# Kernel tuning notes

Measured on AMD Instinct MI355X. Metric: run time of the kernel, lower is better.

## Reference

```python
import jax, jax.numpy as jnp
import numpy as np

B, T, D = 4, 2048, 2048
N_HEADS, N_KV = 16, 4
HEAD_DIM = D // N_HEADS  # 128
N_REP = N_HEADS // N_KV
THETA = 10000.0


def _rope_cos_sin(seq_len, dim, theta):
    inv_freq = 1.0 / (theta ** (jnp.arange(0, dim, 2, dtype=jnp.float32) / dim))
    t = jnp.arange(seq_len, dtype=jnp.float32)
    freqs = jnp.outer(t, inv_freq)               # [T, dim/2]
    emb = jnp.concatenate([freqs, freqs], -1)    # [T, dim]
    return jnp.cos(emb)[None, None], jnp.sin(emb)[None, None]  # [1,1,T,dim]


def _rotate_half(x):
    x1, x2 = jnp.split(x, 2, axis=-1)
    return jnp.concatenate([-x2, x1], axis=-1)


def setup_inputs() -> dict:
    key = jax.random.key(0)
    ks = jax.random.split(key, 5)
    x = jax.random.normal(ks[0], (B, T, D), dtype=jnp.float32)
    # additive causal mask
    causal = jnp.tril(jnp.ones((T, T), dtype=bool))
    mask = jnp.where(causal, 0.0, -1e9).astype(jnp.float32)[None, None]
    s = 0.02
    wq = jax.random.normal(ks[1], (D, N_HEADS * HEAD_DIM), dtype=jnp.float32) * s
    wk = jax.random.normal(ks[2], (D, N_KV * HEAD_DIM), dtype=jnp.float32) * s
    wv = jax.random.normal(ks[3], (D, N_KV * HEAD_DIM), dtype=jnp.float32) * s
    wo = jax.random.normal(ks[4], (D, D), dtype=jnp.float32) * s
    return {"x": x, "mask": mask, "wq": wq, "wk": wk, "wv": wv, "wo": wo}


def reference(x, mask, wq, wk, wv, wo):
    Bc, Tc, _ = x.shape
    q = (x @ wq).reshape(Bc, Tc, N_HEADS, HEAD_DIM).transpose(0, 2, 1, 3)  # [B,H,T,hd]
    k = (x @ wk).reshape(Bc, Tc, N_KV, HEAD_DIM).transpose(0, 2, 1, 3)     # [B,Kv,T,hd]
    v = (x @ wv).reshape(Bc, Tc, N_KV, HEAD_DIM).transpose(0, 2, 1, 3)

    cos, sin = _rope_cos_sin(Tc, HEAD_DIM, THETA)
    q = q * cos + _rotate_half(q) * sin
    k = k * cos + _rotate_half(k) * sin

    # repeat kv heads: [B,Kv,T,hd] -> [B,Kv*n_rep,T,hd]
    k = jnp.repeat(k, N_REP, axis=1)
    v = jnp.repeat(v, N_REP, axis=1)

    scale = HEAD_DIM ** -0.5
    attn = jnp.einsum("bhqd,bhkd->bhqk", q, k) * scale
    attn = attn + mask
    attn = jax.nn.softmax(attn, axis=-1)
    out = jnp.einsum("bhqk,bhkd->bhqd", attn, v)  # [B,H,T,hd]
    out = out.transpose(0, 2, 1, 3).reshape(Bc, Tc, -1)
    return out @ wo
```

## Files before the change

### kernel.cpp

```cpp
#include <hip/hip_runtime.h>

typedef __bf16 bf16;
typedef float  f32x4  __attribute__((ext_vector_type(4)));
typedef float  f32x2  __attribute__((ext_vector_type(2)));
typedef float  f32x16 __attribute__((ext_vector_type(16)));
typedef __bf16 bf16x8 __attribute__((ext_vector_type(8)));
typedef __bf16 bf16x4 __attribute__((ext_vector_type(4)));
typedef unsigned short ushort4_ __attribute__((ext_vector_type(4)));
typedef unsigned int   uint2_   __attribute__((ext_vector_type(2)));

typedef unsigned int __attribute__((address_space(1))) uint_g;
typedef unsigned int __attribute__((address_space(3))) uint_l;

#define DEV __device__ __forceinline__

DEV void gload16(const void* g, void* l) {
  __builtin_amdgcn_global_load_lds((uint_g*)g, (uint_l*)l, 16, 0, 0);
}

#define PHASE_SYNC do { \
  asm volatile("s_barrier" ::: "memory"); \
  asm volatile("s_waitcnt lgkmcnt(0)" ::: "memory"); \
  __builtin_amdgcn_sched_barrier(0); } while (0)

__global__ void k_cvt(const float* __restrict__ in, bf16* __restrict__ out) {
  int i = blockIdx.x * 256 + threadIdx.x;
  f32x4 v = *((const f32x4*)in + i);
  bf16x4 o;
  o[0] = (bf16)v[0]; o[1] = (bf16)v[1]; o[2] = (bf16)v[2]; o[3] = (bf16)v[3];
  *((bf16x4*)out + i) = o;
}

__global__ void k_transpose_cvt(const float* __restrict__ in, bf16* __restrict__ out,
                                int K, int N) {
  __shared__ bf16 tile[64][65];
  int n0 = blockIdx.x * 64, k0 = blockIdx.y * 64;
  int tx = threadIdx.x & 63, ty = threadIdx.x >> 6;
#pragma unroll
  for (int r = 0; r < 64; r += 4)
    tile[r + ty][tx] = (bf16)in[(size_t)(k0 + r + ty) * N + n0 + tx];
  __syncthreads();
#pragma unroll
  for (int r = 0; r < 64; r += 4)
    out[(size_t)(n0 + r + ty) * K + k0 + tx] = tile[tx][r + ty];
}

__global__ void k_rope_tab(f32x2* __restrict__ tab) {
  int idx = blockIdx.x * 256 + threadIdx.x;
  int t = idx >> 6, i = idx & 63;
  float inv = powf(10000.f, -(float)i * (1.f / 64.f));
  float ang = (float)t * inv;
  f32x2 cs; cs[0] = cosf(ang); cs[1] = sinf(ang);
  tab[idx] = cs;
}

template <int MODE>
__global__ __launch_bounds__(512, 2) void k_gemm256(const bf16* __restrict__ A,
                                                    const bf16* __restrict__ Bt,
                                                    void* __restrict__ Cq,
                                                    bf16* __restrict__ Ck,
                                                    bf16* __restrict__ Cv,
                                                    int K) {
  __shared__ bf16 Asm[2][256 * 64];
  __shared__ bf16 Bsm[2][256 * 64];
  const int tid = threadIdx.x;
  const int w = tid >> 6, l = tid & 63, lr = l & 15, lg = l >> 4;
  const int wr = w >> 2, wc = w & 3;
  const int bn = blockIdx.x, bm = blockIdx.y;

  const int srow = tid >> 3;
  const int scb = ((tid & 7) << 4) ^ ((srow & 7) << 4);
  const bf16* Ag = A  + ((size_t)(bm * 256) + srow) * K;
  const bf16* Bg = Bt + ((size_t)(bn * 256) + srow) * K;
  const int ldsbase = w << 10;

  auto stA = [&](int buf, int s, int k0) {
    gload16((const char*)Ag + ((size_t)(s * 64) * K + k0) * 2 + scb,
            (char*)&Asm[buf][0] + s * 8192 + ldsbase);
  };
  auto stB = [&](int buf, int s, int k0) {
    gload16((const char*)Bg + ((size_t)(s * 64) * K + k0) * 2 + scb,
            (char*)&Bsm[buf][0] + s * 8192 + ldsbase);
  };
  auto ldA = [&](int buf, int mf, int kk) -> bf16x8 {
    int row = wr * 128 + mf * 16 + lr;
    return *(const bf16x8*)((const char*)&Asm[buf][0] + row * 128 +
                            ((kk * 64 + lg * 16) ^ ((lr & 7) << 4)));
  };
  auto ldB = [&](int buf, int nf, int kk) -> bf16x8 {
    int row = wc * 64 + nf * 16 + lr;
    return *(const bf16x8*)((const char*)&Bsm[buf][0] + row * 128 +
                            ((kk * 64 + lg * 16) ^ ((lr & 7) << 4)));
  };

  f32x4 acc[8][4] = {};
  const int nt = K >> 6;

#pragma unroll
  for (int s = 0; s < 4; s++) { stA(0, s, 0); stB(0, s, 0); }
  asm volatile("s_waitcnt vmcnt(0)" ::: "memory");
  __syncthreads();

#pragma unroll 1
  for (int t = 0; t < nt; t++) {
    const int cur = t & 1, nxt = cur ^ 1;
    const int kn = (t + 1) << 6;
    const bool pre = (t + 1 < nt);
    bf16x8 a0[4][2], a1[4][2], b0[2][2], b1[2][2];

#pragma unroll
    for (int mf = 0; mf < 4; mf++) { a0[mf][0] = ldA(cur, mf, 0); a0[mf][1] = ldA(cur, mf, 1); }
#pragma unroll
    for (int nf = 0; nf < 2; nf++) { b0[nf][0] = ldB(cur, nf, 0); b0[nf][1] = ldB(cur, nf, 1); }
    if (pre) { stA(nxt, 0, kn); stA(nxt, 1, kn); stA(nxt, 2, kn); }
    PHASE_SYNC;
    __builtin_amdgcn_s_setprio(1);
#pragma unroll
    for (int mf = 0; mf < 4; mf++)
#pragma unroll
      for (int nf = 0; nf < 2; nf++)
#pragma unroll
        for (int kk = 0; kk < 2; kk++)
          acc[mf][nf] = __builtin_amdgcn_mfma_f32_16x16x32_bf16(a0[mf][kk], b0[nf][kk], acc[mf][nf], 0, 0, 0);
    __builtin_amdgcn_s_setprio(0);

#pragma unroll
    for (int nf = 0; nf < 2; nf++) { b1[nf][0] = ldB(cur, nf + 2, 0); b1[nf][1] = ldB(cur, nf + 2, 1); }
    if (pre) { stA(nxt, 3, kn); stB(nxt, 0, kn); stB(nxt, 1, kn); }
    PHASE_SYNC;
    __builtin_amdgcn_s_setprio(1);
#pragma unroll
    for (int mf = 0; mf < 4; mf++)
#pragma unroll
      for (int nf = 0; nf < 2; nf++)
#pragma unroll
        for (int kk = 0; kk < 2; kk++)
          acc[mf][nf + 2] = __builtin_amdgcn_mfma_f32_16x16x32_bf16(a0[mf][kk], b1[nf][kk], acc[mf][nf + 2], 0, 0, 0);
    __builtin_amdgcn_s_setprio(0);

#pragma unroll
    for (int mf = 0; mf < 4; mf++) { a1[mf][0] = ldA(cur, mf + 4, 0); a1[mf][1] = ldA(cur, mf + 4, 1); }
    if (pre) { stB(nxt, 2, kn); stB(nxt, 3, kn); }
    PHASE_SYNC;
    __builtin_amdgcn_s_setprio(1);
#pragma unroll
    for (int mf = 0; mf < 4; mf++)
#pragma unroll
      for (int nf = 0; nf < 2; nf++)
#pragma unroll
        for (int kk = 0; kk < 2; kk++)
          acc[mf + 4][nf] = __builtin_amdgcn_mfma_f32_16x16x32_bf16(a1[mf][kk], b0[nf][kk], acc[mf + 4][nf], 0, 0, 0);
    __builtin_amdgcn_s_setprio(0);

    __builtin_amdgcn_s_setprio(1);
#pragma unroll
    for (int mf = 0; mf < 4; mf++)
#pragma unroll
      for (int nf = 0; nf < 2; nf++)
#pragma unroll
        for (int kk = 0; kk < 2; kk++)
          acc[mf + 4][nf + 2] = __builtin_amdgcn_mfma_f32_16x16x32_bf16(a1[mf][kk], b1[nf][kk], acc[mf + 4][nf + 2], 0, 0, 0);
    __builtin_amdgcn_s_setprio(0);
    asm volatile("s_waitcnt vmcnt(0)" ::: "memory");
    asm volatile("s_barrier" ::: "memory");
  }

#pragma unroll
  for (int mf = 0; mf < 8; mf++) {
    const int rowb = bm * 256 + wr * 128 + mf * 16 + lg * 4;
#pragma unroll
    for (int nf = 0; nf < 4; nf++) {
      const int col = bn * 256 + wc * 64 + nf * 16 + lr;
      if constexpr (MODE == 0) {
        float* Cf = (float*)Cq;
#pragma unroll
        for (int j = 0; j < 4; j++)
          Cf[(size_t)(rowb + j) * 2048 + col] = acc[mf][nf][j];
      } else {
        if (bn < 8) {
          bf16* Cb = (bf16*)Cq;
#pragma unroll
          for (int j = 0; j < 4; j++)
            Cb[(size_t)(rowb + j) * 2048 + col] = (bf16)acc[mf][nf][j];
        } else if (bn < 10) {
          int kcol = col - 2048;
#pragma unroll
          for (int j = 0; j < 4; j++)
            Ck[(size_t)(rowb + j) * 512 + kcol] = (bf16)acc[mf][nf][j];
        } else {
          int vcol = col - 2560;
          int kv = vcol >> 7, d = vcol & 127;
          int bb = rowb >> 11, t0 = rowb & 2047;
          size_t off = ((size_t)((bb * 4 + kv) * 128 + d)) * 2048 + t0;
          ushort4_ pk;
#pragma unroll
          for (int j = 0; j < 4; j++)
            pk[j] = __builtin_bit_cast(unsigned short, (bf16)acc[mf][nf][j]);
          *(ushort4_*)(Cv + off) = pk;
        }
      }
    }
  }
}

template <int LOGNH>
__global__ void k_rope(const bf16* __restrict__ in, bf16* __restrict__ out,
                       const f32x2* __restrict__ tab, float scl) {
  const int NH = 1 << LOGNH;
  int idx = blockIdx.x * 256 + threadIdx.x;
  int dq = idx & 15;
  int h = (idx >> 4) & (NH - 1);
  int bt = idx >> (4 + LOGNH);
  int t = bt & 2047;
  int d0 = dq * 4;
  const bf16* pin = in + (size_t)bt * (NH * 128) + h * 128;
  bf16x4 x1 = *(const bf16x4*)(pin + d0);
  bf16x4 x2 = *(const bf16x4*)(pin + 64 + d0);
  bf16x4 o1, o2;
#pragma unroll
  for (int j = 0; j < 4; j++) {
    f32x2 cs = tab[t * 64 + d0 + j];
    float c1 = cs[0] * scl, s1 = cs[1] * scl;
    float a = (float)x1[j], c2 = (float)x2[j];
    o1[j] = (bf16)(a * c1 - c2 * s1);
    o2[j] = (bf16)(c2 * c1 + a * s1);
  }
  int b = bt >> 11;
  bf16* pout = out + (((size_t)(b << LOGNH) + h) * 2048 + t) * 128;
  *(bf16x4*)(pout + d0) = o1;
  *(bf16x4*)(pout + 64 + d0) = o2;
}

__global__ __launch_bounds__(256, 2) void k_attn(const bf16* __restrict__ Qraw,
                                                 const bf16* __restrict__ Kb,
                                                 const bf16* __restrict__ Vt,
                                                 bf16* __restrict__ AO,
                                                 const f32x2* __restrict__ tab,
                                                 float qscl) {
  __shared__ bf16 Ks[2][64 * 128];
  __shared__ bf16 Vs[2][128 * 64];
  __shared__ bf16 Ps[4][32 * 64];
  const int tid = threadIdx.x, w = tid >> 6, l = tid & 63;
  const int bh = blockIdx.y, b = bh >> 4, h = bh & 15, kvh = h >> 2;
  const int pi = blockIdx.x;
  const int l31 = l & 31, hi = l >> 5;

  const bf16* Kh = Kb + (size_t)(b * 4 + kvh) * (2048 * 128);
  const bf16* Vh = Vt + (size_t)(b * 4 + kvh) * (128 * 2048);
  char* Pw = (char*)&Ps[w][0] + l31 * 128;
  const int qsw = (l & 7) << 4;

  auto stage = [&](int kv0, int buf) {
#pragma unroll
    for (int i = 0; i < 4; i++) {
      int krow = w * 16 + i * 4 + (l >> 4);
      int kcb = ((l & 15) * 16) ^ ((krow & 7) << 4);
      gload16(Kh + (size_t)(kv0 + krow) * 128 + (kcb >> 1), (bf16*)&Ks[buf][0] + w * 2048 + i * 512);
      int vrow = w * 32 + i * 8 + (l >> 3);
      int vcb = ((l & 7) * 16) ^ ((vrow & 7) << 4);
      gload16(Vh + (size_t)vrow * 2048 + kv0 + (vcb >> 1), (bf16*)&Vs[buf][0] + w * 2048 + i * 512);
    }
  };

#pragma unroll 1
  for (int ph = 0; ph < 2; ph++) {
    const int q0 = (ph ? (15 - pi) : pi) * 128;
    const int nt = q0 / 64 + 2;
    const int qw0 = q0 + w * 32;
    const int qg = qw0 + l31;

    bf16x8 qf[8];
    {
      const bf16* qp = Qraw + ((size_t)(b * 2048 + qg)) * 2048 + h * 128 + hi * 8;
      const f32x2* tb = tab + qg * 64 + hi * 8;
      bf16x8 xr[8];
#pragma unroll
      for (int kk = 0; kk < 8; kk++) xr[kk] = *(const bf16x8*)(qp + kk * 16);
#pragma unroll
      for (int kk = 0; kk < 4; kk++) {
#pragma unroll
        for (int j = 0; j < 8; j++) {
          f32x2 cs = tb[kk * 16 + j];
          float a = (float)xr[kk][j], c2 = (float)xr[kk + 4][j];
          qf[kk][j]     = (bf16)((a * cs[0] - c2 * cs[1]) * qscl);
          qf[kk + 4][j] = (bf16)((c2 * cs[0] + a * cs[1]) * qscl);
        }
      }
    }

    f32x16 ot[4] = {};
    float m_ = -3e38f, l_ = 0.f;

    int cur = 0;
    stage(0, 0);
    __syncthreads();

#pragma unroll 1
    for (int t = 0; t < nt; t++) {
      const int kv0 = t * 64;
      if (t + 1 < nt) stage(kv0 + 64, cur ^ 1);

      if (kv0 <= qw0 + 31) {
        f32x16 st[2] = {};
        __builtin_amdgcn_s_setprio(1);
#pragma unroll
        for (int nb = 0; nb < 2; nb++) {
          const int row = nb * 32 + l31;
          const char* kbase = (const char*)&Ks[cur][0] + row * 256;
#pragma unroll
          for (int kk = 0; kk < 8; kk++) {
            bf16x8 kf = *(const bf16x8*)(kbase + ((kk * 32 + hi * 16) ^ qsw));
            st[nb] = __builtin_amdgcn_mfma_f32_32x32x16_bf16(kf, qf[kk], st[nb], 0, 0, 0);
          }
        }
        __builtin_amdgcn_s_setprio(0);

        if (kv0 + 63 > qw0) {
#pragma unroll
          for (int nb = 0; nb < 2; nb++) {
            const int kvb = kv0 + nb * 32 + 4 * hi;
#pragma unroll
            for (int r = 0; r < 16; r++) {
              int kg = kvb + (r & 3) + 8 * (r >> 2);
              if (kg > qg) st[nb][r] = -3e38f;
            }
          }
        }
        float mx = -3e38f;
#pragma unroll
        for (int nb = 0; nb < 2; nb++)
#pragma unroll
          for (int r = 0; r < 16; r++) mx = fmaxf(mx, st[nb][r]);
        mx = fmaxf(mx, __shfl_xor(mx, 32));
        if (!__all(mx - m_ <= 8.f)) {
          float mnew = fmaxf(m_, mx);
          float corr = exp2f(m_ - mnew);
          m_ = mnew; l_ *= corr;
#pragma unroll
          for (int dt = 0; dt < 4; dt++)
#pragma unroll
            for (int r = 0; r < 16; r++) ot[dt][r] *= corr;
        }
        float ls = 0.f;
#pragma unroll
        for (int nb = 0; nb < 2; nb++)
#pragma unroll
          for (int a = 0; a < 4; a++) {
            uint2_ pr;
#pragma unroll
            for (int half = 0; half < 2; half++) {
              float p0 = exp2f(st[nb][4 * a + 2 * half] - m_);
              float p1 = exp2f(st[nb][4 * a + 2 * half + 1] - m_);
              ls += p0 + p1;
              unsigned short b0 = __builtin_bit_cast(unsigned short, (bf16)p0);
              unsigned short b1 = __builtin_bit_cast(unsigned short, (bf16)p1);
              pr[half] = (unsigned int)b0 | ((unsigned int)b1 << 16);
            }
            *(uint2_*)(Pw + ((nb * 64 + a * 16 + hi * 8) ^ qsw)) = pr;
          }
        ls += __shfl_xor(ls, 32);
        l_ += ls;

        __builtin_amdgcn_s_setprio(1);
#pragma unroll
        for (int kb = 0; kb < 4; kb++) {
          bf16x8 pb = *(const bf16x8*)(Pw + ((kb * 32 + hi * 16) ^ qsw));
#pragma unroll
          for (int dt = 0; dt < 4; dt++) {
            const int vrow = dt * 32 + l31;
            const char* vp = (const char*)&Vs[cur][0] + vrow * 128 + ((kb * 32 + hi * 16) ^ qsw);
            bf16x8 vf = *(const bf16x8*)vp;
            ot[dt] = __builtin_amdgcn_mfma_f32_32x32x16_bf16(vf, pb, ot[dt], 0, 0, 0);
          }
        }
        __builtin_amdgcn_s_setprio(0);
      }

      __syncthreads();
      cur ^= 1;
    }

    const float inv = 1.f / l_;
    bf16* op = AO + ((size_t)b * 2048 + qg) * 2048 + h * 128;
#pragma unroll
    for (int dt = 0; dt < 4; dt++)
#pragma unroll
      for (int rq = 0; rq < 4; rq++) {
        ushort4_ pk;
#pragma unroll
        for (int j = 0; j < 4; j++)
          pk[j] = __builtin_bit_cast(unsigned short, (bf16)(ot[dt][rq * 4 + j] * inv));
        *(ushort4_*)(op + dt * 32 + rq * 8 + hi * 4) = pk;
      }
  }
}

extern "C" void kernel_launch(void* const* d_in, const int* in_sizes, int n_in,
                              void* d_out, int out_size, void* d_ws, size_t ws_size,
                              hipStream_t stream) {
  const float* x  = (const float*)d_in[0];
  const float* wq = (const float*)d_in[2];
  const float* wk = (const float*)d_in[3];
  const float* wv = (const float*)d_in[4];
  const float* wo = (const float*)d_in[5];

  char* p = (char*)d_ws;
  auto alloc = [&](size_t bytes) { char* r = p; p += (bytes + 255) & ~(size_t)255; return r; };
  bf16*  xb     = (bf16*)alloc(8192ull * 2048 * 2);
  bf16*  wqkvT  = (bf16*)alloc(3072ull * 2048 * 2);
  bf16*  woT    = (bf16*)alloc(2048ull * 2048 * 2);
  f32x2* tab    = (f32x2*)alloc(2048ull * 64 * 8);
  bf16*  Qtmp   = (bf16*)alloc(8192ull * 2048 * 2);
  bf16*  Ktmp   = (bf16*)alloc(8192ull * 512 * 2);
  bf16*  Kr     = (bf16*)alloc(8192ull * 512 * 2);
  bf16*  Vr     = (bf16*)alloc(8192ull * 512 * 2);

  k_cvt<<<16384, 256, 0, stream>>>(x, xb);
  k_transpose_cvt<<<dim3(32, 32), 256, 0, stream>>>(wq, wqkvT, 2048, 2048);
  k_transpose_cvt<<<dim3(8, 32),  256, 0, stream>>>(wk, wqkvT + 2048ull * 2048, 2048, 512);
  k_transpose_cvt<<<dim3(8, 32),  256, 0, stream>>>(wv, wqkvT + 2560ull * 2048, 2048, 512);
  k_transpose_cvt<<<dim3(32, 32), 256, 0, stream>>>(wo, woT, 2048, 2048);
  k_rope_tab<<<512, 256, 0, stream>>>(tab);

  k_gemm256<1><<<dim3(12, 32), 512, 0, stream>>>(xb, wqkvT, Qtmp, Ktmp, Vr, 2048);

  const float qscl = 0.08838834764831845f * 1.4426950408889634f;
  k_rope<2><<<2048, 256, 0, stream>>>(Ktmp, Kr, tab, 1.0f);

  k_attn<<<dim3(8, 64), 256, 0, stream>>>(Qtmp, Kr, Vr, Qtmp, tab, qscl);

  k_gemm256<0><<<dim3(8, 32), 512, 0, stream>>>(Qtmp, woT, d_out, nullptr, nullptr, 2048);
}
```

Baseline: 336.7 us.

## Reorder GEMM main loop into four k-split phases with partial vmcnt waits

The 256x256 bf16 GEMM main loop is restructured into four phases, each over a half-K slice. Each phase loads fragments for four M-subtiles by four N-subtiles, which cuts live fragment registers, and spreads the next-tile global->LDS prefetches across the phases. It also replaces the full vmcnt(0) drain with vmcnt(2) partial waits plus extra barriers, and changes launch bounds from 2 to 1 blocks per CU to give the compiler more register headroom. The extra barriers and the lower occupancy bound may add stalls, and the partial waits must still cover the LDS data each phase reads.

```diff
diff --git a/kernel.cpp b/kernel.cpp
--- a/kernel.cpp
+++ b/kernel.cpp
@@ -18,6 +18,7 @@
   __builtin_amdgcn_global_load_lds((uint_g*)g, (uint_l*)l, 16, 0, 0);
 }
 
+#define SBAR  asm volatile("s_barrier" ::: "memory")
 #define PHASE_SYNC do { \
   asm volatile("s_barrier" ::: "memory"); \
   asm volatile("s_waitcnt lgkmcnt(0)" ::: "memory"); \
@@ -55,7 +56,7 @@
 }
 
 template <int MODE>
-__global__ __launch_bounds__(512, 2) void k_gemm256(const bf16* __restrict__ A,
+__global__ __launch_bounds__(512, 1) void k_gemm256(const bf16* __restrict__ A,
                                                     const bf16* __restrict__ Bt,
                                                     void* __restrict__ Cq,
                                                     bf16* __restrict__ Ck,
@@ -106,63 +107,65 @@
     const int cur = t & 1, nxt = cur ^ 1;
     const int kn = (t + 1) << 6;
     const bool pre = (t + 1 < nt);
-    bf16x8 a0[4][2], a1[4][2], b0[2][2], b1[2][2];
-
-#pragma unroll
-    for (int mf = 0; mf < 4; mf++) { a0[mf][0] = ldA(cur, mf, 0); a0[mf][1] = ldA(cur, mf, 1); }
-#pragma unroll
-    for (int nf = 0; nf < 2; nf++) { b0[nf][0] = ldB(cur, nf, 0); b0[nf][1] = ldB(cur, nf, 1); }
-    if (pre) { stA(nxt, 0, kn); stA(nxt, 1, kn); stA(nxt, 2, kn); }
+    bf16x8 a[4], b[4];
+
+#pragma unroll
+    for (int mf = 0; mf < 4; mf++) a[mf] = ldA(cur, mf, 0);
+#pragma unroll
+    for (int nf = 0; nf < 4; nf++) b[nf] = ldB(cur, nf, 0);
+    if (pre) { stA(nxt, 0, kn); stA(nxt, 2, kn); }
     PHASE_SYNC;
     __builtin_amdgcn_s_setprio(1);
 #pragma unroll
     for (int mf = 0; mf < 4; mf++)
 #pragma unroll
-      for (int nf = 0; nf < 2; nf++)
-#pragma unroll
-        for (int kk = 0; kk < 2; kk++)
-          acc[mf][nf] = __builtin_amdgcn_mfma_f32_16x16x32_bf16(a0[mf][kk], b0[nf][kk], acc[mf][nf], 0, 0, 0);
+      for (int nf = 0; nf < 4; nf++)
+        acc[mf][nf] = __builtin_amdgcn_mfma_f32_16x16x32_bf16(a[mf], b[nf], acc[mf][nf], 0, 0, 0);
     __builtin_amdgcn_s_setprio(0);
-
-#pragma unroll
-    for (int nf = 0; nf < 2; nf++) { b1[nf][0] = ldB(cur, nf + 2, 0); b1[nf][1] = ldB(cur, nf + 2, 1); }
-    if (pre) { stA(nxt, 3, kn); stB(nxt, 0, kn); stB(nxt, 1, kn); }
+    asm volatile("s_waitcnt vmcnt(2)" ::: "memory");
+    SBAR;
+
+#pragma unroll
+    for (int mf = 0; mf < 4; mf++) a[mf] = ldA(cur, mf + 4, 0);
+    if (pre) { stB(nxt, 0, kn); stB(nxt, 1, kn); }
     PHASE_SYNC;
     __builtin_amdgcn_s_setprio(1);
 #pragma unroll
     for (int mf = 0; mf < 4; mf++)
 #pragma unroll
-      for (int nf = 0; nf < 2; nf++)
-#pragma unroll
-        for (int kk = 0; kk < 2; kk++)
-          acc[mf][nf + 2] = __builtin_amdgcn_mfma_f32_16x16x32_bf16(a0[mf][kk], b1[nf][kk], acc[mf][nf + 2], 0, 0, 0);
+      for (int nf = 0; nf < 4; nf++)
+        acc[mf + 4][nf] = __builtin_amdgcn_mfma_f32_16x16x32_bf16(a[mf], b[nf], acc[mf + 4][nf], 0, 0, 0);
     __builtin_amdgcn_s_setprio(0);
-
-#pragma unroll
-    for (int mf = 0; mf < 4; mf++) { a1[mf][0] = ldA(cur, mf + 4, 0); a1[mf][1] = ldA(cur, mf + 4, 1); }
+    SBAR;
+
+#pragma unroll
+    for (int mf = 0; mf < 4; mf++) a[mf] = ldA(cur, mf, 1);
+#pragma unroll
+    for (int nf = 0; nf < 4; nf++) b[nf] = ldB(cur, nf, 1);
     if (pre) { stB(nxt, 2, kn); stB(nxt, 3, kn); }
     PHASE_SYNC;
     __builtin_amdgcn_s_setprio(1);
 #pragma unroll
     for (int mf = 0; mf < 4; mf++)
 #pragma unroll
-      for (int nf = 0; nf < 2; nf++)
-#pragma unroll
-        for (int kk = 0; kk < 2; kk++)
-          acc[mf + 4][nf] = __builtin_amdgcn_mfma_f32_16x16x32_bf16(a1[mf][kk], b0[nf][kk], acc[mf + 4][nf], 0, 0, 0);
+      for (int nf = 0; nf < 4; nf++)
+        acc[mf][nf] = __builtin_amdgcn_mfma_f32_16x16x32_bf16(a[mf], b[nf], acc[mf][nf], 0, 0, 0);
     __builtin_amdgcn_s_setprio(0);
-
+    SBAR;
+
+#pragma unroll
+    for (int mf = 0; mf < 4; mf++) a[mf] = ldA(cur, mf + 4, 1);
+    if (pre) { stA(nxt, 1, kn); stA(nxt, 3, kn); }
+    PHASE_SYNC;
     __builtin_amdgcn_s_setprio(1);
 #pragma unroll
     for (int mf = 0; mf < 4; mf++)
 #pragma unroll
-      for (int nf = 0; nf < 2; nf++)
-#pragma unroll
-        for (int kk = 0; kk < 2; kk++)
-          acc[mf + 4][nf + 2] = __builtin_amdgcn_mfma_f32_16x16x32_bf16(a1[mf][kk], b1[nf][kk], acc[mf + 4][nf + 2], 0, 0, 0);
+      for (int nf = 0; nf < 4; nf++)
+        acc[mf + 4][nf] = __builtin_amdgcn_mfma_f32_16x16x32_bf16(a[mf], b[nf], acc[mf + 4][nf], 0, 0, 0);
     __builtin_amdgcn_s_setprio(0);
-    asm volatile("s_waitcnt vmcnt(0)" ::: "memory");
-    asm volatile("s_barrier" ::: "memory");
+    asm volatile("s_waitcnt vmcnt(2)" ::: "memory");
+    SBAR;
   }
 
 #pragma unroll
```

Result: slower. 344.7 us (+2.4%).

## Double per-wave query rows in attention to reuse K/V fragments across two MFMA tiles

Applied to the files above, without the earlier changes.

Each wave now handles 64 query rows (two 32-row MFMA tiles) instead of 32, so every K and V fragment read from LDS feeds two MFMAs. Block query tile grows from 128 to 256 rows and the grid halves to 4x64 blocks, with causal pairing adjusted to 7-pi. Register pressure roughly doubles for accumulators, so launch bounds drop to one block per SM and the P scratch buffer doubles. The change trades occupancy and grid parallelism (256 blocks) for higher arithmetic intensity per LDS load.

```diff
diff --git a/kernel.cpp b/kernel.cpp
--- a/kernel.cpp
+++ b/kernel.cpp
@@ -231,7 +231,7 @@
   *(bf16x4*)(pout + 64 + d0) = o2;
 }
 
-__global__ __launch_bounds__(256, 2) void k_attn(const bf16* __restrict__ Qraw,
+__global__ __launch_bounds__(256, 1) void k_attn(const bf16* __restrict__ Qraw,
                                                  const bf16* __restrict__ Kb,
                                                  const bf16* __restrict__ Vt,
                                                  bf16* __restrict__ AO,
@@ -239,7 +239,7 @@
                                                  float qscl) {
   __shared__ bf16 Ks[2][64 * 128];
   __shared__ bf16 Vs[2][128 * 64];
-  __shared__ bf16 Ps[4][32 * 64];
+  __shared__ bf16 Ps[4][64 * 64];
   const int tid = threadIdx.x, w = tid >> 6, l = tid & 63;
   const int bh = blockIdx.y, b = bh >> 4, h = bh & 15, kvh = h >> 2;
   const int pi = blockIdx.x;
@@ -247,7 +247,7 @@
 
   const bf16* Kh = Kb + (size_t)(b * 4 + kvh) * (2048 * 128);
   const bf16* Vh = Vt + (size_t)(b * 4 + kvh) * (128 * 2048);
-  char* Pw = (char*)&Ps[w][0] + l31 * 128;
+  char* Pw = (char*)&Ps[w][0];
   const int qsw = (l & 7) << 4;
 
   auto stage = [&](int kv0, int buf) {
@@ -264,13 +264,15 @@
 
 #pragma unroll 1
   for (int ph = 0; ph < 2; ph++) {
-    const int q0 = (ph ? (15 - pi) : pi) * 128;
-    const int nt = q0 / 64 + 2;
-    const int qw0 = q0 + w * 32;
-    const int qg = qw0 + l31;
-
-    bf16x8 qf[8];
-    {
+    const int q0 = (ph ? (7 - pi) : pi) * 256;
+    const int nt = q0 / 64 + 4;
+    const int q0w = q0 + w * 64;
+    const int qg0 = q0w + l31, qg1 = q0w + 32 + l31;
+
+    bf16x8 qf[2][8];
+#pragma unroll
+    for (int nq = 0; nq < 2; nq++) {
+      const int qg = q0w + nq * 32 + l31;
       const bf16* qp = Qraw + ((size_t)(b * 2048 + qg)) * 2048 + h * 128 + hi * 8;
       const f32x2* tb = tab + qg * 64 + hi * 8;
       bf16x8 xr[8];
@@ -282,14 +284,14 @@
         for (int j = 0; j < 8; j++) {
           f32x2 cs = tb[kk * 16 + j];
           float a = (float)xr[kk][j], c2 = (float)xr[kk + 4][j];
-          qf[kk][j]     = (bf16)((a * cs[0] - c2 * cs[1]) * qscl);
-          qf[kk + 4][j] = (bf16)((c2 * cs[0] + a * cs[1]) * qscl);
+          qf[nq][kk][j]     = (bf16)((a * cs[0] - c2 * cs[1]) * qscl);
+          qf[nq][kk + 4][j] = (bf16)((c2 * cs[0] + a * cs[1]) * qscl);
         }
       }
     }
 
-    f32x16 ot[4] = {};
-    float m_ = -3e38f, l_ = 0.f;
+    f32x16 ot[2][4] = {};
+    float m_[2] = {-3e38f, -3e38f}, l_[2] = {0.f, 0.f};
 
     int cur = 0;
     stage(0, 0);
@@ -300,8 +302,8 @@
       const int kv0 = t * 64;
       if (t + 1 < nt) stage(kv0 + 64, cur ^ 1);
 
-      if (kv0 <= qw0 + 31) {
-        f32x16 st[2] = {};
+      if (kv0 <= q0w + 63) {
+        f32x16 st[2][2] = {};
         __builtin_amdgcn_s_setprio(1);
 #pragma unroll
         for (int nb = 0; nb < 2; nb++) {
@@ -310,67 +312,85 @@
 #pragma unroll
           for (int kk = 0; kk < 8; kk++) {
             bf16x8 kf = *(const bf16x8*)(kbase + ((kk * 32 + hi * 16) ^ qsw));
-            st[nb] = __builtin_amdgcn_mfma_f32_32x32x16_bf16(kf, qf[kk], st[nb], 0, 0, 0);
+            st[nb][0] = __builtin_amdgcn_mfma_f32_32x32x16_bf16(kf, qf[0][kk], st[nb][0], 0, 0, 0);
+            st[nb][1] = __builtin_amdgcn_mfma_f32_32x32x16_bf16(kf, qf[1][kk], st[nb][1], 0, 0, 0);
           }
         }
         __builtin_amdgcn_s_setprio(0);
 
-        if (kv0 + 63 > qw0) {
+        if (kv0 + 63 > q0w) {
 #pragma unroll
           for (int nb = 0; nb < 2; nb++) {
             const int kvb = kv0 + nb * 32 + 4 * hi;
 #pragma unroll
             for (int r = 0; r < 16; r++) {
-              int kg = kvb + (r & 3) + 8 * (r >> 2);
-              if (kg > qg) st[nb][r] = -3e38f;
+              const int kg = kvb + (r & 3) + 8 * (r >> 2);
+              if (kg > qg0) st[nb][0][r] = -3e38f;
+              if (kg > qg1) st[nb][1][r] = -3e38f;
             }
           }
         }
-        float mx = -3e38f;
-#pragma unroll
-        for (int nb = 0; nb < 2; nb++)
-#pragma unroll
-          for (int r = 0; r < 16; r++) mx = fmaxf(mx, st[nb][r]);
-        mx = fmaxf(mx, __shfl_xor(mx, 32));
-        if (!__all(mx - m_ <= 8.f)) {
-          float mnew = fmaxf(m_, mx);
-          float corr = exp2f(m_ - mnew);
-          m_ = mnew; l_ *= corr;
-#pragma unroll
-          for (int dt = 0; dt < 4; dt++)
-#pragma unroll
-            for (int r = 0; r < 16; r++) ot[dt][r] *= corr;
-        }
-        float ls = 0.f;
-#pragma unroll
-        for (int nb = 0; nb < 2; nb++)
-#pragma unroll
-          for (int a = 0; a < 4; a++) {
-            uint2_ pr;
-#pragma unroll
-            for (int half = 0; half < 2; half++) {
-              float p0 = exp2f(st[nb][4 * a + 2 * half] - m_);
-              float p1 = exp2f(st[nb][4 * a + 2 * half + 1] - m_);
-              ls += p0 + p1;
-              unsigned short b0 = __builtin_bit_cast(unsigned short, (bf16)p0);
-              unsigned short b1 = __builtin_bit_cast(unsigned short, (bf16)p1);
-              pr[half] = (unsigned int)b0 | ((unsigned int)b1 << 16);
+        float mx[2];
+#pragma unroll
+        for (int nq = 0; nq < 2; nq++) {
+          float m = -3e38f;
+#pragma unroll
+          for (int nb = 0; nb < 2; nb++)
+#pragma unroll
+            for (int r = 0; r < 16; r++) m = fmaxf(m, st[nb][nq][r]);
+          m = fmaxf(m, __shfl_xor(m, 32));
+          mx[nq] = m;
+        }
+        if (!__all(fmaxf(mx[0] - m_[0], mx[1] - m_[1]) <= 8.f)) {
+#pragma unroll
+          for (int nq = 0; nq < 2; nq++) {
+            float mnew = fmaxf(m_[nq], mx[nq]);
+            float corr = exp2f(m_[nq] - mnew);
+            m_[nq] = mnew; l_[nq] *= corr;
+#pragma unroll
+            for (int dt = 0; dt < 4; dt++)
+#pragma unroll
+              for (int r = 0; r < 16; r++) ot[nq][dt][r] *= corr;
+          }
+        }
+#pragma unroll
+        for (int nq = 0; nq < 2; nq++) {
+          float ls = 0.f;
+          const int qloc = nq * 32 + l31;
+#pragma unroll
+          for (int nb = 0; nb < 2; nb++)
+#pragma unroll
+            for (int a = 0; a < 4; a++) {
+              uint2_ pr;
+#pragma unroll
+              for (int half = 0; half < 2; half++) {
+                float p0 = exp2f(st[nb][nq][4 * a + 2 * half] - m_[nq]);
+                float p1 = exp2f(st[nb][nq][4 * a + 2 * half + 1] - m_[nq]);
+                ls += p0 + p1;
+                unsigned short b0 = __builtin_bit_cast(unsigned short, (bf16)p0);
+                unsigned short b1 = __builtin_bit_cast(unsigned short, (bf16)p1);
+                pr[half] = (unsigned int)b0 | ((unsigned int)b1 << 16);
+              }
+              *(uint2_*)(Pw + qloc * 128 + ((nb * 64 + a * 16 + hi * 8) ^ qsw)) = pr;
             }
-            *(uint2_*)(Pw + ((nb * 64 + a * 16 + hi * 8) ^ qsw)) = pr;
-          }
-        ls += __shfl_xor(ls, 32);
-        l_ += ls;
+          ls += __shfl_xor(ls, 32);
+          l_[nq] += ls;
+        }
 
         __builtin_amdgcn_s_setprio(1);
 #pragma unroll
         for (int kb = 0; kb < 4; kb++) {
-          bf16x8 pb = *(const bf16x8*)(Pw + ((kb * 32 + hi * 16) ^ qsw));
+          bf16x8 pb[2];
+#pragma unroll
+          for (int nq = 0; nq < 2; nq++)
+            pb[nq] = *(const bf16x8*)(Pw + (nq * 32 + l31) * 128 + ((kb * 32 + hi * 16) ^ qsw));
 #pragma unroll
           for (int dt = 0; dt < 4; dt++) {
             const int vrow = dt * 32 + l31;
             const char* vp = (const char*)&Vs[cur][0] + vrow * 128 + ((kb * 32 + hi * 16) ^ qsw);
             bf16x8 vf = *(const bf16x8*)vp;
-            ot[dt] = __builtin_amdgcn_mfma_f32_32x32x16_bf16(vf, pb, ot[dt], 0, 0, 0);
+            ot[0][dt] = __builtin_amdgcn_mfma_f32_32x32x16_bf16(vf, pb[0], ot[0][dt], 0, 0, 0);
+            ot[1][dt] = __builtin_amdgcn_mfma_f32_32x32x16_bf16(vf, pb[1], ot[1][dt], 0, 0, 0);
           }
         }
         __builtin_amdgcn_s_setprio(0);
@@ -380,18 +400,22 @@
       cur ^= 1;
     }
 
-    const float inv = 1.f / l_;
-    bf16* op = AO + ((size_t)b * 2048 + qg) * 2048 + h * 128;
-#pragma unroll
-    for (int dt = 0; dt < 4; dt++)
-#pragma unroll
-      for (int rq = 0; rq < 4; rq++) {
-        ushort4_ pk;
-#pragma unroll
-        for (int j = 0; j < 4; j++)
-          pk[j] = __builtin_bit_cast(unsigned short, (bf16)(ot[dt][rq * 4 + j] * inv));
-        *(ushort4_*)(op + dt * 32 + rq * 8 + hi * 4) = pk;
-      }
+#pragma unroll
+    for (int nq = 0; nq < 2; nq++) {
+      const float inv = 1.f / l_[nq];
+      const int qg = q0w + nq * 32 + l31;
+      bf16* op = AO + ((size_t)b * 2048 + qg) * 2048 + h * 128;
+#pragma unroll
+      for (int dt = 0; dt < 4; dt++)
+#pragma unroll
+        for (int rq = 0; rq < 4; rq++) {
+          ushort4_ pk;
+#pragma unroll
+          for (int j = 0; j < 4; j++)
+            pk[j] = __builtin_bit_cast(unsigned short, (bf16)(ot[nq][dt][rq * 4 + j] * inv));
+          *(ushort4_*)(op + dt * 32 + rq * 8 + hi * 4) = pk;
+        }
+    }
   }
 }
 
@@ -427,7 +451,7 @@
   const float qscl = 0.08838834764831845f * 1.4426950408889634f;
   k_rope<2><<<2048, 256, 0, stream>>>(Ktmp, Kr, tab, 1.0f);
 
-  k_attn<<<dim3(8, 64), 256, 0, stream>>>(Qtmp, Kr, Vr, Qtmp, tab, qscl);
+  k_attn<<<dim3(4, 64), 256, 0, stream>>>(Qtmp, Kr, Vr, Qtmp, tab, qscl);
 
   k_gemm256<0><<<dim3(8, 32), 512, 0, stream>>>(Qtmp, woT, d_out, nullptr, nullptr, 2048);
 }
```

Result: slower. 390.3 us (+15.9%).
